# Optimization experiments

Hardware: AMD Instinct MI355X
Metric: run time of the kernel (lower is better)

Reference implementation:

```python
import jax, jax.numpy as jnp
import numpy as np

S = 17          # number of segment ids (0 = background, skipped)
MIN_H = 100.0   # HomographySmoothLoss.min_segment_pixels
MIN_V = 50.0    # ObjectVarianceLoss.min_segment_pixels
SUPPRESS = 0.1  # BoundaryAwareSmoothLoss.boundary_suppress


def _maxpool3(x):
    # torch F.max_pool2d(k=3, stride=1, pad=1) pads with -inf
    return jax.lax.reduce_window(x, -jnp.inf, jax.lax.max,
                                 (1, 1, 3, 3), (1, 1, 1, 1),
                                 ((0, 0), (0, 0), (1, 1), (1, 1)))


def _boundary_map(masks):
    lab = masks.astype(jnp.float32)[:, None]  # (B,1,H,W)
    dil = _maxpool3(lab)
    ero = -_maxpool3(-lab)
    return (dil != ero).astype(jnp.float32)


def _nearest(x, Ho, Wo):
    # torch F.interpolate(mode='nearest'): src = floor(dst * in/out)
    H, W = x.shape[-2], x.shape[-1]
    yi = (jnp.arange(Ho) * H) // Ho
    xi = (jnp.arange(Wo) * W) // Wo
    return x[..., yi, :][..., :, xi]


def _conv3(x, k):
    return jax.lax.conv_general_dilated(x, k, (1, 1), ((1, 1), (1, 1)),
                                        dimension_numbers=('NCHW', 'OIHW', 'NCHW'))


def _segment_losses(flow, masks):
    # Vectorized replacement of per-(batch,segment) python loops:
    # accumulate per-segment moments with segment_sum, then batched 3x3
    # normal-equation solves (equivalent to torch.lstsq affine fit).
    B, _, H, W = flow.shape
    NS = B * S
    xs = jnp.broadcast_to(jnp.arange(W, dtype=jnp.float32)[None, None, :], (B, H, W)).reshape(-1)
    ys = jnp.broadcast_to(jnp.arange(H, dtype=jnp.float32)[None, :, None], (B, H, W)).reshape(-1)
    u = flow[:, 0].reshape(-1)
    v = flow[:, 1].reshape(-1)
    seg = masks.reshape(-1)
    bidx = jnp.repeat(jnp.arange(B, dtype=jnp.int32), H * W)
    idx = bidx * S + seg                                  # global segment id
    ones = jnp.ones_like(xs)
    feats = jnp.stack([ones, xs, ys, xs * xs, xs * ys, ys * ys,
                       u, v, u * u, v * v, xs * u, ys * u, xs * v, ys * v], axis=1)
    sums = jax.ops.segment_sum(feats, idx, num_segments=NS)  # (NS,14)
    (n, Sx, Sy, Sxx, Sxy, Syy, Su, Sv, Suu, Svv,
     Sxu, Syu, Sxv, Syv) = [sums[:, i] for i in range(14)]
    segids = jnp.tile(jnp.arange(S), B)

    # ---- homography loss: per-segment affine least-squares fit ----
    valid_h = (segids != 0) & (n >= MIN_H)
    ATA = jnp.stack([jnp.stack([Sxx, Sxy, Sx], -1),
                     jnp.stack([Sxy, Syy, Sy], -1),
                     jnp.stack([Sx, Sy, n], -1)], axis=1)   # (NS,3,3)
    eye3 = jnp.eye(3, dtype=flow.dtype)
    ATA = jnp.where(valid_h[:, None, None], ATA, eye3)      # keep solve nonsingular
    ATb = jnp.stack([jnp.stack([Sxu, Sxv], -1),
                     jnp.stack([Syu, Syv], -1),
                     jnp.stack([Su, Sv], -1)], axis=1)      # (NS,3,2)
    ATb = jnp.where(valid_h[:, None, None], ATb, 0.0)
    params = jnp.linalg.solve(ATA, ATb)                     # (NS,3,2): [a,b,c] for u and v
    p = params[idx]                                         # (BHW,3,2) gather per pixel
    pred_u = xs * p[:, 0, 0] + ys * p[:, 1, 0] + p[:, 2, 0]
    pred_v = xs * p[:, 0, 1] + ys * p[:, 1, 1] + p[:, 2, 1]
    res = jnp.sqrt((u - pred_u) ** 2 + (v - pred_v) ** 2)
    res_mean = jax.ops.segment_sum(res, idx, num_segments=NS) / jnp.maximum(n, 1.0)
    nh = jnp.maximum(jnp.sum(valid_h), 1)
    homog = jnp.sum(res_mean * valid_h) / nh

    # ---- object variance loss (unbiased var, matches torch .var()) ----
    valid_v = (segids != 0) & (n >= MIN_V)
    nsafe = jnp.maximum(n, 2.0)
    var_u = (Suu - Su * Su / nsafe) / (nsafe - 1.0)
    var_v = (Svv - Sv * Sv / nsafe) / (nsafe - 1.0)
    nv = jnp.maximum(jnp.sum(valid_v), 1)
    ovar = jnp.sum((var_u + var_v) * valid_v) / nv
    return homog, ovar


def setup_inputs():
    key = jax.random.key(0)
    k1, k2, k3 = jax.random.split(key, 3)
    B, H, W = 8, 512, 1024
    flow = jax.random.normal(k1, (B, 2, H, W), jnp.float32)
    masks = jax.random.randint(k2, (B, H, W), 0, S).astype(jnp.int32)
    images = jax.random.uniform(k3, (B, 3, H, W), jnp.float32)
    return {"flow": flow, "masks": masks, "images": images}


def reference(flow, masks, images):
    boundary = _boundary_map(masks)                         # (B,1,H,W)
    homog, ovar = _segment_losses(flow, masks)

    # ---- boundary sharpness (sobel on flow magnitude) ----
    sobel_x = jnp.array([[-1., 0., 1.], [-2., 0., 2.], [-1., 0., 1.]], jnp.float32).reshape(1, 1, 3, 3)
    sobel_y = jnp.array([[-1., -2., -1.], [0., 0., 0.], [1., 2., 1.]], jnp.float32).reshape(1, 1, 3, 3)
    flow_mag = jnp.sqrt(jnp.sum(flow ** 2, axis=1, keepdims=True))
    fg = jnp.abs(_conv3(flow_mag, sobel_x)) + jnp.abs(_conv3(flow_mag, sobel_y))
    fg = fg / (jnp.max(fg) + 1e-6)
    bn = boundary / (jnp.max(boundary) + 1e-6)
    sharp = jnp.mean(bn * (1.0 - fg))

    # ---- boundary-aware edge-weighted smoothness ----
    flow_dx = flow[:, :, :, 1:] - flow[:, :, :, :-1]
    flow_dy = flow[:, :, 1:, :] - flow[:, :, :-1, :]
    g = jnp.mean(images, axis=1, keepdims=True)
    wx = jnp.exp(-jnp.abs(g[:, :, :, 1:] - g[:, :, :, :-1]) * 10.0)
    wy = jnp.exp(-jnp.abs(g[:, :, 1:, :] - g[:, :, :-1, :]) * 10.0)
    bx = _nearest(boundary, wx.shape[2], wx.shape[3])
    by = _nearest(boundary, wy.shape[2], wy.shape[3])
    wx = wx * (1.0 - (1.0 - SUPPRESS) * bx)
    wy = wy * (1.0 - (1.0 - SUPPRESS) * by)
    smooth = jnp.mean(jnp.abs(flow_dx) * wx) + jnp.mean(jnp.abs(flow_dy) * wy)

    # weights all 1.0; order: homography, boundary_sharpness, object_variance, boundary_smooth
    return jnp.stack([homog, sharp, ovar, smooth])
```

## Files before the change

### kernel.cpp

```cpp
#include <hip/hip_runtime.h>
#include <math.h>

#define BB 8
#define HH 512
#define WW 1024
#define HW (HH * WW)
#define NPIX (BB * HW)
#define NSEG 16
#define SUPPRESS 0.1f


__device__ __forceinline__ float wave_sum(float t) {
    #pragma unroll
    for (int off = 32; off > 0; off >>= 1) t += __shfl_down(t, off);
    return t;
}

#define REP8(M) M(0) M(1) M(2) M(3) M(4) M(5) M(6) M(7)

__global__ __launch_bounds__(64) void moments_kernel(
    const float* __restrict__ flow,
    const int*   __restrict__ masks,
    double* __restrict__ moments4)
{
    __shared__ float bins[9984];

    const int lane = threadIdx.x;
    const int bid  = blockIdx.x;
    const int colg = bid & 15;
    const int rowg = (bid >> 4) & 7;
    const int b    = bid >> 7;
    const int par  = bid & 3;

    const int c0 = colg * 64;
    const int r0 = rowg * 64;

    const float* fu = flow + (long long)b * (2LL * HW);
    const float* fv = fu + HW;
    const int*   mk = masks + (long long)b * HW;
    const int*   mrow = mk + r0 * WW + c0 + lane;
    const float* urow = fu + r0 * WW + c0 + lane;
    const float* vrow = fv + r0 * WW + c0 + lane;

    #pragma unroll
    for (int i = 0; i < 39; ++i)
        *(float4*)&bins[i * 256 + lane * 4] = make_float4(0.f, 0.f, 0.f, 0.f);

    int   m0 = mrow[0];
    float u0 = urow[0], v0 = vrow[0];
    int   m1 = mrow[WW];
    float u1 = urow[WW], v1 = vrow[WW];

    #pragma unroll 1
    for (int r = 0; r < 64; r += 2) {
        const int o2 = ((r + 2) & 63) * WW;
        const int o3 = ((r + 3) & 63) * WW;
        const int   m2 = mrow[o2];
        const float u2 = urow[o2], v2 = vrow[o2];
        const int   m3 = mrow[o3];
        const float u3 = urow[o3], v3 = vrow[o3];

        {
            const float y = (float)(r0 + r);
            float* bp = &bins[m0 * 576 + lane];
            float b0 = bp[0],   b1 = bp[64],  b2 = bp[128];
            float b3 = bp[192], b4 = bp[256], b5 = bp[320];
            float b6 = bp[384], b7 = bp[448], b8 = bp[512];
            b0 += 1.f;
            b1 += y;
            b2 = fmaf(y, y, b2);
            b3 += u0;
            b4 += v0;
            b5 = fmaf(u0, u0, b5);
            b6 = fmaf(v0, v0, b6);
            b7 = fmaf(y, u0, b7);
            b8 = fmaf(y, v0, b8);
            bp[0] = b0;   bp[64] = b1;  bp[128] = b2;
            bp[192] = b3; bp[256] = b4; bp[320] = b5;
            bp[384] = b6; bp[448] = b7; bp[512] = b8;
        }
        {
            const float y = (float)(r0 + r + 1);
            float* bp = &bins[m1 * 576 + lane];
            float b0 = bp[0],   b1 = bp[64],  b2 = bp[128];
            float b3 = bp[192], b4 = bp[256], b5 = bp[320];
            float b6 = bp[384], b7 = bp[448], b8 = bp[512];
            b0 += 1.f;
            b1 += y;
            b2 = fmaf(y, y, b2);
            b3 += u1;
            b4 += v1;
            b5 = fmaf(u1, u1, b5);
            b6 = fmaf(v1, v1, b6);
            b7 = fmaf(y, u1, b7);
            b8 = fmaf(y, v1, b8);
            bp[0] = b0;   bp[64] = b1;  bp[128] = b2;
            bp[192] = b3; bp[256] = b4; bp[320] = b5;
            bp[384] = b6; bp[448] = b7; bp[512] = b8;
        }
        m0 = m2; u0 = u2; v0 = v2;
        m1 = m3; u1 = u3; v1 = v3;
    }

    const unsigned long long SRC = 0x84736543210100ULL;
    const unsigned long long PW  = 0x01010000012010ULL;
    double* cell = moments4 + par * 1792 + b * 224;
    #pragma unroll 1
    for (int rp = 0; rp < 4; ++rp) {
        const int p   = rp * 64 + lane;
        const int act = (p < 224);
        const int pc  = act ? p : 0;
        const int segm = pc / 14;
        const int feat = pc - segm * 14;
        const int srcb = (int)((SRC >> (4 * feat)) & 15);
        const int pw   = (int)((PW  >> (4 * feat)) & 15);
        const float* bp = &bins[(segm + 1) * 576 + srcb * 64];
        float acc = 0.f;
        #pragma unroll 8
        for (int l0 = 0; l0 < 64; ++l0) {
            const int l = (l0 + lane) & 63;
            const float xv = (float)(c0 + l);
            const float w = (pw == 0) ? 1.f : ((pw == 1) ? xv : xv * xv);
            acc = fmaf(bp[l], w, acc);
        }
        if (act) atomicAdd(&cell[segm * 14 + feat], (double)acc);
    }
}

__global__ __launch_bounds__(256) void stencil_kernel(
    const float* __restrict__ flow,
    const int*   __restrict__ masks,
    const float* __restrict__ images,
    double* __restrict__ scal64,
    unsigned* __restrict__ maxfg64)
{
    __shared__ float         sm[4][1032];
    __shared__ unsigned char smask[4][1032];
    __shared__ float         sg[3][1024];
    __shared__ float         wred[4][5];

    const int tid = threadIdx.x;
    const int lane = tid & 63;
    const long long base = (long long)blockIdx.x * 2048;
    const int b  = (int)(base >> 19);
    const int h0 = (int)((base & (HW - 1)) >> 10);

    const float* fu = flow + (long long)b * (2LL * HW);
    const float* fv = fu + HW;
    const int*   mk = masks + (long long)b * HW;
    const float* i0 = images + (long long)b * (3LL * HW);
    const float* i1 = i0 + HW;
    const float* i2 = i1 + HW;

    const int c4 = tid * 4;
    #pragma unroll
    for (int r = 0; r < 4; ++r) {
        const int gr = h0 - 1 + r;
        const int mr = gr < 0 ? 0 : (gr > HH - 1 ? HH - 1 : gr);
        const int4 mv = *(const int4*)&mk[mr * WW + c4];
        uchar4 mb;
        mb.x = (unsigned char)mv.x; mb.y = (unsigned char)mv.y;
        mb.z = (unsigned char)mv.z; mb.w = (unsigned char)mv.w;
        *(uchar4*)&smask[r][4 + c4] = mb;

        float4 u4 = make_float4(0.f, 0.f, 0.f, 0.f);
        float4 v4 = make_float4(0.f, 0.f, 0.f, 0.f);
        if (gr >= 0 && gr <= HH - 1) {
            u4 = *(const float4*)&fu[gr * WW + c4];
            v4 = *(const float4*)&fv[gr * WW + c4];
        }
        float4 m4;
        m4.x = sqrtf(u4.x * u4.x + v4.x * v4.x);
        m4.y = sqrtf(u4.y * u4.y + v4.y * v4.y);
        m4.z = sqrtf(u4.z * u4.z + v4.z * v4.z);
        m4.w = sqrtf(u4.w * u4.w + v4.w * v4.w);
        *(float4*)&sm[r][4 + c4] = m4;
    }
    #pragma unroll
    for (int r = 0; r < 3; ++r) {
        const int gr = h0 + r;
        float4 g4 = make_float4(0.f, 0.f, 0.f, 0.f);
        if (gr <= HH - 1) {
            const float4 a  = *(const float4*)&i0[gr * WW + c4];
            const float4 bq = *(const float4*)&i1[gr * WW + c4];
            const float4 c  = *(const float4*)&i2[gr * WW + c4];
            g4.x = (a.x + bq.x + c.x) * (1.f / 3.f);
            g4.y = (a.y + bq.y + c.y) * (1.f / 3.f);
            g4.z = (a.z + bq.z + c.z) * (1.f / 3.f);
            g4.w = (a.w + bq.w + c.w) * (1.f / 3.f);
        }
        *(float4*)&sg[r][c4] = g4;
    }
    if (tid < 4) {
        const int gr = h0 - 1 + tid;
        const int mr = gr < 0 ? 0 : (gr > HH - 1 ? HH - 1 : gr);
        smask[tid][3]    = (unsigned char)mk[mr * WW + 0];
        smask[tid][1028] = (unsigned char)mk[mr * WW + WW - 1];
        sm[tid][3] = 0.f;
        sm[tid][1028] = 0.f;
    }
    __syncthreads();

    float a_dx = 0.f, a_dy = 0.f, a_sb = 0.f, a_sbf = 0.f, mfg = 0.f;

    #pragma unroll
    for (int it = 0; it < 8; ++it) {
        const int idx = it * 256 + tid;
        const int lr = idx >> 10;
        const int w  = idx & 1023;
        const int h  = h0 + lr;
        const int cc = 4 + w;

        const int segc = smask[lr + 1][cc];
        int bnd = (smask[lr][cc - 1] != segc) | (smask[lr][cc] != segc) |
                  (smask[lr][cc + 1] != segc) |
                  (smask[lr + 1][cc - 1] != segc) | (smask[lr + 1][cc + 1] != segc) |
                  (smask[lr + 2][cc - 1] != segc) | (smask[lr + 2][cc] != segc) |
                  (smask[lr + 2][cc + 1] != segc);

        const float t00 = sm[lr][cc - 1],     t01 = sm[lr][cc],     t02 = sm[lr][cc + 1];
        const float t10 = sm[lr + 1][cc - 1],                       t12 = sm[lr + 1][cc + 1];
        const float t20 = sm[lr + 2][cc - 1], t21 = sm[lr + 2][cc], t22 = sm[lr + 2][cc + 1];
        const float fgx = (t02 - t00) + 2.f * (t12 - t10) + (t22 - t20);
        const float fgy = (t20 + 2.f * t21 + t22) - (t00 + 2.f * t01 + t02);
        const float fgraw = fabsf(fgx) + fabsf(fgy);
        mfg = fmaxf(mfg, fgraw);
        if (bnd) { a_sb += 1.f; a_sbf += fgraw; }

        const int hw = h * WW + w;
        const float u = fu[hw], v = fv[hw];
        const float g0 = sg[lr][w];
        if (w < WW - 1) {
            const float wgt = expf(-fabsf(sg[lr][w + 1] - g0) * 10.f) * (bnd ? SUPPRESS : 1.f);
            a_dx += (fabsf(fu[hw + 1] - u) + fabsf(fv[hw + 1] - v)) * wgt;
        }
        if (h < HH - 1) {
            const float wgt = expf(-fabsf(sg[lr + 1][w] - g0) * 10.f) * (bnd ? SUPPRESS : 1.f);
            a_dy += (fabsf(fu[hw + WW] - u) + fabsf(fv[hw + WW] - v)) * wgt;
        }
    }

    for (int off = 32; off > 0; off >>= 1) {
        a_dx += __shfl_down(a_dx, off);
        a_dy += __shfl_down(a_dy, off);
        a_sb += __shfl_down(a_sb, off);
        a_sbf += __shfl_down(a_sbf, off);
        mfg = fmaxf(mfg, __shfl_down(mfg, off));
    }
    if (lane == 0) {
        const int wv = tid >> 6;
        wred[wv][0] = a_dx; wred[wv][1] = a_dy; wred[wv][2] = a_sb;
        wred[wv][3] = a_sbf; wred[wv][4] = mfg;
    }
    __syncthreads();
    if (tid == 0) {
        float dx = 0.f, dy = 0.f, sb = 0.f, sbf = 0.f, mf = 0.f;
        for (int i = 0; i < 4; ++i) {
            dx += wred[i][0]; dy += wred[i][1]; sb += wred[i][2];
            sbf += wred[i][3]; mf = fmaxf(mf, wred[i][4]);
        }
        const int sl = blockIdx.x & 63;
        atomicAdd(&scal64[sl * 4 + 0], (double)dx);
        atomicAdd(&scal64[sl * 4 + 1], (double)dy);
        atomicAdd(&scal64[sl * 4 + 2], (double)sb);
        atomicAdd(&scal64[sl * 4 + 3], (double)sbf);
        atomicMax(&maxfg64[sl], __float_as_uint(mf));
    }
}

__global__ __launch_bounds__(128) void solve_kernel(
    const double* __restrict__ moments4,
    float* __restrict__ params,
    int* __restrict__ valid,
    float* __restrict__ out)
{
    const int i = threadIdx.x;
    double m[14];
    #pragma unroll
    for (int k = 0; k < 14; ++k) {
        double s = 0.0;
        #pragma unroll
        for (int par = 0; par < 4; ++par) s += moments4[par * 1792 + i * 14 + k];
        m[k] = s;
    }
    const double n = m[0];
    const int vh = (n >= 100.0) ? 1 : 0;
    float p[6] = {0.f, 0.f, 0.f, 0.f, 0.f, 0.f};
    if (vh) {
        double A[3][3] = {{m[3], m[4], m[1]},
                          {m[4], m[5], m[2]},
                          {m[1], m[2], n}};
        double Bm[3][2] = {{m[10], m[12]},
                           {m[11], m[13]},
                           {m[6],  m[7]}};
        for (int k = 0; k < 3; ++k) {
            int piv = k; double mx = fabs(A[k][k]);
            for (int r = k + 1; r < 3; ++r) {
                double a = fabs(A[r][k]);
                if (a > mx) { mx = a; piv = r; }
            }
            if (piv != k) {
                for (int c = 0; c < 3; ++c) { double t = A[k][c]; A[k][c] = A[piv][c]; A[piv][c] = t; }
                for (int c = 0; c < 2; ++c) { double t = Bm[k][c]; Bm[k][c] = Bm[piv][c]; Bm[piv][c] = t; }
            }
            const double inv = 1.0 / A[k][k];
            for (int r = k + 1; r < 3; ++r) {
                const double f = A[r][k] * inv;
                for (int c = k; c < 3; ++c) A[r][c] -= f * A[k][c];
                Bm[r][0] -= f * Bm[k][0];
                Bm[r][1] -= f * Bm[k][1];
            }
        }
        double X[3][2];
        for (int c = 0; c < 2; ++c) {
            X[2][c] = Bm[2][c] / A[2][2];
            X[1][c] = (Bm[1][c] - A[1][2] * X[2][c]) / A[1][1];
            X[0][c] = (Bm[0][c] - A[0][1] * X[1][c] - A[0][2] * X[2][c]) / A[0][0];
        }
        p[0] = (float)X[0][0]; p[1] = (float)X[1][0]; p[2] = (float)X[2][0];
        p[3] = (float)X[0][1]; p[4] = (float)X[1][1]; p[5] = (float)X[2][1];
    }
    valid[i] = vh;
    for (int c = 0; c < 6; ++c) params[i * 6 + c] = p[c];

    const int vv = (n >= 50.0) ? 1 : 0;
    double var = 0.0;
    if (vv) {
        const double ns = (n > 2.0) ? n : 2.0;
        const double var_u = (m[8] - m[6] * m[6] / ns) / (ns - 1.0);
        const double var_v = (m[9] - m[7] * m[7] / ns) / (ns - 1.0);
        var = var_u + var_v;
    }
    __shared__ double svar[128];
    __shared__ int scnt[128];
    svar[i] = var; scnt[i] = vv;
    __syncthreads();
    for (int s = 64; s > 0; s >>= 1) {
        if (i < s) { svar[i] += svar[i + s]; scnt[i] += scnt[i + s]; }
        __syncthreads();
    }
    if (i == 0) out[2] = (float)(svar[0] / (double)(scnt[0] > 1 ? scnt[0] : 1));
}

__global__ __launch_bounds__(256) void pass2_kernel(
    const float* __restrict__ flow,
    const int*   __restrict__ masks,
    const float* __restrict__ params,
    double* __restrict__ res4)
{
    __shared__ float sp[17 * 6];

    const long long base = (long long)blockIdx.x * 4096;
    const int b      = (int)(base >> 19);
    const int hwbase = (int)(base & (HW - 1));
    const int tid    = threadIdx.x;
    const int lane   = tid & 63;

    if (tid < 6) sp[tid] = 0.f;
    if (tid < 96) sp[6 + tid] = params[b * 96 + tid];
    __syncthreads();

    const float* fu = flow + (long long)b * (2LL * HW);
    const float* fv = fu + HW;
    const int*   mk = masks + (long long)b * HW;

#define DECLR(i) float r_##i = 0.f;
    REP8(DECLR)
#define DECLR2(i) float q_##i = 0.f;
    REP8(DECLR2)

    #pragma unroll
    for (int it = 0; it < 4; ++it) {
        const int i4 = hwbase + it * 1024 + tid * 4;
        const int4   m4 = *(const int4*)&mk[i4];
        const float4 u4 = *(const float4*)&fu[i4];
        const float4 v4 = *(const float4*)&fv[i4];
        const int segs[4] = {m4.x, m4.y, m4.z, m4.w};
        const float us[4] = {u4.x, u4.y, u4.z, u4.w};
        const float vs[4] = {v4.x, v4.y, v4.z, v4.w};
        #pragma unroll
        for (int j = 0; j < 4; ++j) {
            const int seg = segs[j];
            const float* pf = &sp[seg * 6];
            const int hw = i4 + j;
            const float x = (float)(hw & 1023), y = (float)((hw & (HW - 1)) >> 10);
            const float du = us[j] - (x * pf[0] + y * pf[1] + pf[2]);
            const float dv = vs[j] - (x * pf[3] + y * pf[4] + pf[5]);
            const float r = sqrtf(du * du + dv * dv);
            const int sr = seg - 1;
#define STEPR(i) r_##i += (sr == i) ? r : 0.f;
            REP8(STEPR)
#define STEPR2(i) q_##i += (sr == 8 + i) ? r : 0.f;
            REP8(STEPR2)
        }
    }

    const int par = blockIdx.x & 3;
    double* rb = &res4[par * 128 + b * 16];
#define FINR(i) { const float s = wave_sum(r_##i); \
    if (lane == 0) atomicAdd(rb + i, (double)s); }
    REP8(FINR)
#define FINR2(i) { const float s = wave_sum(q_##i); \
    if (lane == 0) atomicAdd(rb + 8 + i, (double)s); }
    REP8(FINR2)
}

__global__ __launch_bounds__(128) void final_kernel(
    const double* __restrict__ moments4,
    const double* __restrict__ res4,
    const int*    __restrict__ valid,
    const double* __restrict__ scal64,
    const unsigned* __restrict__ maxfg64,
    float* __restrict__ out)
{
    const int i = threadIdx.x;
    double n = 0.0, rs = 0.0;
    #pragma unroll
    for (int par = 0; par < 4; ++par) {
        n  += moments4[par * 1792 + i * 14];
        rs += res4[par * 128 + i];
    }
    const int vh = valid[i];
    const double rm = vh ? rs / (n > 1.0 ? n : 1.0) : 0.0;
    __shared__ double sr[128];
    __shared__ int sc[128];
    sr[i] = rm; sc[i] = vh;
    __syncthreads();
    for (int s = 64; s > 0; s >>= 1) {
        if (i < s) { sr[i] += sr[i + s]; sc[i] += sc[i + s]; }
        __syncthreads();
    }
    if (i == 0) {
        out[0] = (float)(sr[0] / (double)(sc[0] > 1 ? sc[0] : 1));
        double dx = 0.0, dy = 0.0, sb = 0.0, sbf = 0.0;
        float mf = 0.f;
        for (int k = 0; k < 64; ++k) {
            dx += scal64[k * 4 + 0]; dy += scal64[k * 4 + 1];
            sb += scal64[k * 4 + 2]; sbf += scal64[k * 4 + 3];
            mf = fmaxf(mf, __uint_as_float(maxfg64[k]));
        }
        const double maxfg = (double)mf;
        const double maxb = (sb > 0.0) ? 1.0 : 0.0;
        out[1] = (float)((sb - sbf / (maxfg + 1e-6)) / (maxb + 1e-6) / (double)NPIX);
        const double smooth = dx / (double)(2LL * BB * HH * (WW - 1)) +
                              dy / (double)(2LL * BB * (HH - 1) * WW);
        out[3] = (float)smooth;
    }
}

extern "C" void kernel_launch(void* const* d_in, const int* in_sizes, int n_in,
                              void* d_out, int out_size, void* d_ws, size_t ws_size,
                              hipStream_t stream)
{
    const float* flow   = (const float*)d_in[0];
    const int*   masks  = (const int*)d_in[1];
    const float* images = (const float*)d_in[2];
    float* out = (float*)d_out;

    char* ws = (char*)d_ws;
    double*   moments4 = (double*)(ws);
    double*   res4     = (double*)(ws + 57344);
    double*   scal64   = (double*)(ws + 61440);
    unsigned* maxfg64  = (unsigned*)(ws + 63488);
    float*    params   = (float*)(ws + 63744);
    int*      valid    = (int*)(ws + 66816);

    hipMemsetAsync(d_ws, 0, 67584, stream);

    moments_kernel<<<dim3(1024), dim3(64), 0, stream>>>(flow, masks, moments4);
    stencil_kernel<<<dim3(NPIX / 2048), dim3(256), 0, stream>>>(
        flow, masks, images, scal64, maxfg64);
    solve_kernel<<<dim3(1), dim3(128), 0, stream>>>(moments4, params, valid, out);
    pass2_kernel<<<dim3(NPIX / 4096), dim3(256), 0, stream>>>(
        flow, masks, params, res4);
    final_kernel<<<dim3(1), dim3(128), 0, stream>>>(
        moments4, res4, valid, scal64, maxfg64, out);
}
```

Measured before the change: 119.7 us.

## Process four adjacent pixels per thread in stencil, reusing register-held flow and gray

The stencil loop now handles four consecutive columns per thread over two rows. The mask and magnitude neighbourhoods are read once into registers, and the mask bytes are packed into 64-bit words. The flow and gray values already loaded for the shared-memory fill are reused for the dx/dy terms, with a small shared edge buffer for the right neighbour, instead of re-reading flow from global memory per pixel. A launch-bounds occupancy hint is also added. The cost is higher register pressure per thread and less parallel slack per pixel.

```diff
diff --git a/kernel.cpp b/kernel.cpp
--- a/kernel.cpp
+++ b/kernel.cpp
@@ -127,7 +127,7 @@
     }
 }
 
-__global__ __launch_bounds__(256) void stencil_kernel(
+__global__ __launch_bounds__(256, 4) void stencil_kernel(
     const float* __restrict__ flow,
     const int*   __restrict__ masks,
     const float* __restrict__ images,
@@ -137,6 +137,8 @@
     __shared__ float         sm[4][1032];
     __shared__ unsigned char smask[4][1032];
     __shared__ float         sg[3][1024];
+    __shared__ float         ue[2][260];
+    __shared__ float         ve[2][260];
     __shared__ float         wred[4][5];
 
     const int tid = threadIdx.x;
@@ -153,6 +155,8 @@
     const float* i2 = i1 + HW;
 
     const int c4 = tid * 4;
+    float4 ur0, ur1, ur2, vr0, vr1, vr2;
+
     #pragma unroll
     for (int r = 0; r < 4; ++r) {
         const int gr = h0 - 1 + r;
@@ -175,7 +179,11 @@
         m4.z = sqrtf(u4.z * u4.z + v4.z * v4.z);
         m4.w = sqrtf(u4.w * u4.w + v4.w * v4.w);
         *(float4*)&sm[r][4 + c4] = m4;
-    }
+        if (r == 1) { ur0 = u4; vr0 = v4; }
+        else if (r == 2) { ur1 = u4; vr1 = v4; }
+        else if (r == 3) { ur2 = u4; vr2 = v4; }
+    }
+    float4 gr0, gr1, gr2;
     #pragma unroll
     for (int r = 0; r < 3; ++r) {
         const int gr = h0 + r;
@@ -190,7 +198,10 @@
             g4.w = (a.w + bq.w + c.w) * (1.f / 3.f);
         }
         *(float4*)&sg[r][c4] = g4;
-    }
+        if (r == 0) gr0 = g4; else if (r == 1) gr1 = g4; else gr2 = g4;
+    }
+    ue[0][tid] = ur0.x; ve[0][tid] = vr0.x;
+    ue[1][tid] = ur1.x; ve[1][tid] = vr1.x;
     if (tid < 4) {
         const int gr = h0 - 1 + tid;
         const int mr = gr < 0 ? 0 : (gr > HH - 1 ? HH - 1 : gr);
@@ -204,39 +215,65 @@
     float a_dx = 0.f, a_dy = 0.f, a_sb = 0.f, a_sbf = 0.f, mfg = 0.f;
 
     #pragma unroll
-    for (int it = 0; it < 8; ++it) {
-        const int idx = it * 256 + tid;
-        const int lr = idx >> 10;
-        const int w  = idx & 1023;
-        const int h  = h0 + lr;
-        const int cc = 4 + w;
-
-        const int segc = smask[lr + 1][cc];
-        int bnd = (smask[lr][cc - 1] != segc) | (smask[lr][cc] != segc) |
-                  (smask[lr][cc + 1] != segc) |
-                  (smask[lr + 1][cc - 1] != segc) | (smask[lr + 1][cc + 1] != segc) |
-                  (smask[lr + 2][cc - 1] != segc) | (smask[lr + 2][cc] != segc) |
-                  (smask[lr + 2][cc + 1] != segc);
-
-        const float t00 = sm[lr][cc - 1],     t01 = sm[lr][cc],     t02 = sm[lr][cc + 1];
-        const float t10 = sm[lr + 1][cc - 1],                       t12 = sm[lr + 1][cc + 1];
-        const float t20 = sm[lr + 2][cc - 1], t21 = sm[lr + 2][cc], t22 = sm[lr + 2][cc + 1];
-        const float fgx = (t02 - t00) + 2.f * (t12 - t10) + (t22 - t20);
-        const float fgy = (t20 + 2.f * t21 + t22) - (t00 + 2.f * t01 + t02);
-        const float fgraw = fabsf(fgx) + fabsf(fgy);
-        mfg = fmaxf(mfg, fgraw);
-        if (bnd) { a_sb += 1.f; a_sbf += fgraw; }
-
-        const int hw = h * WW + w;
-        const float u = fu[hw], v = fv[hw];
-        const float g0 = sg[lr][w];
-        if (w < WW - 1) {
-            const float wgt = expf(-fabsf(sg[lr][w + 1] - g0) * 10.f) * (bnd ? SUPPRESS : 1.f);
-            a_dx += (fabsf(fu[hw + 1] - u) + fabsf(fv[hw + 1] - v)) * wgt;
-        }
-        if (h < HH - 1) {
-            const float wgt = expf(-fabsf(sg[lr + 1][w] - g0) * 10.f) * (bnd ? SUPPRESS : 1.f);
-            a_dy += (fabsf(fu[hw + WW] - u) + fabsf(fv[hw + WW] - v)) * wgt;
+    for (int lr = 0; lr < 2; ++lr) {
+        const int h = h0 + lr;
+        float a[3][6];
+        unsigned long long kw[3];
+        #pragma unroll
+        for (int r = 0; r < 3; ++r) {
+            const int rr = lr + r;
+            const float4 own = *(const float4*)&sm[rr][4 + c4];
+            a[r][0] = sm[rr][3 + c4];
+            a[r][1] = own.x; a[r][2] = own.y; a[r][3] = own.z; a[r][4] = own.w;
+            a[r][5] = sm[rr][8 + c4];
+            const unsigned mpk = *(const unsigned*)&smask[rr][4 + c4];
+            kw[r] = (unsigned long long)smask[rr][3 + c4]
+                  | ((unsigned long long)mpk << 8)
+                  | ((unsigned long long)smask[rr][8 + c4] << 40);
+        }
+        const float4 gc = (lr == 0) ? gr0 : gr1;
+        const float4 gd4 = (lr == 0) ? gr1 : gr2;
+        const float gRn = (c4 + 4 < WW) ? sg[lr][c4 + 4] : 0.f;
+        const float gval[5] = {gc.x, gc.y, gc.z, gc.w, gRn};
+        const float4 uc4 = (lr == 0) ? ur0 : ur1;
+        const float4 vc4 = (lr == 0) ? vr0 : vr1;
+        const float4 ud4 = (lr == 0) ? ur1 : ur2;
+        const float4 vd4 = (lr == 0) ? vr1 : vr2;
+        const float uc[5] = {uc4.x, uc4.y, uc4.z, uc4.w, ue[lr][tid + 1]};
+        const float vc[5] = {vc4.x, vc4.y, vc4.z, vc4.w, ve[lr][tid + 1]};
+        const float ud[4] = {ud4.x, ud4.y, ud4.z, ud4.w};
+        const float vd[4] = {vd4.x, vd4.y, vd4.z, vd4.w};
+
+        #pragma unroll
+        for (int j = 0; j < 4; ++j) {
+            const int w = c4 + j;
+            const int cseg = (int)((kw[1] >> (8 * (j + 1))) & 255);
+            int bnd = (((kw[0] >> (8 * j)) & 255) != (unsigned)cseg)
+                    | (((kw[0] >> (8 * (j + 1))) & 255) != (unsigned)cseg)
+                    | (((kw[0] >> (8 * (j + 2))) & 255) != (unsigned)cseg)
+                    | (((kw[1] >> (8 * j)) & 255) != (unsigned)cseg)
+                    | (((kw[1] >> (8 * (j + 2))) & 255) != (unsigned)cseg)
+                    | (((kw[2] >> (8 * j)) & 255) != (unsigned)cseg)
+                    | (((kw[2] >> (8 * (j + 1))) & 255) != (unsigned)cseg)
+                    | (((kw[2] >> (8 * (j + 2))) & 255) != (unsigned)cseg);
+
+            const float fgx = (a[0][j + 2] - a[0][j]) + 2.f * (a[1][j + 2] - a[1][j]) +
+                              (a[2][j + 2] - a[2][j]);
+            const float fgy = (a[2][j] + 2.f * a[2][j + 1] + a[2][j + 2]) -
+                              (a[0][j] + 2.f * a[0][j + 1] + a[0][j + 2]);
+            const float fgraw = fabsf(fgx) + fabsf(fgy);
+            mfg = fmaxf(mfg, fgraw);
+            if (bnd) { a_sb += 1.f; a_sbf += fgraw; }
+
+            const float u = uc[j], v = vc[j], g0 = gval[j];
+            if (w < WW - 1) {
+                const float wgt = expf(-fabsf(gval[j + 1] - g0) * 10.f) * (bnd ? SUPPRESS : 1.f);
+                a_dx += (fabsf(uc[j + 1] - u) + fabsf(vc[j + 1] - v)) * wgt;
+            }
+            if (h < HH - 1) {
+                const float wgt = expf(-fabsf(gd4.x * 0.f + ((const float*)&gd4)[j] - g0) * 10.f) * (bnd ? SUPPRESS : 1.f);
+                a_dy += (fabsf(ud[j] - u) + fabsf(vd[j] - v)) * wgt;
+            }
         }
     }
 
```

New measurement: 108.4 us. 1.1x faster.

## Fuse segment-moment histogram and boundary stencil into one sliding-window kernel

Applied to the files above, without the earlier changes.

Merges the per-segment moments kernel and the boundary/smoothness stencil kernel into one 64-thread kernel. Each wave walks 64 rows over a 62-column tile with one-column halos, keeping a 3-row register window and using lane shuffles for horizontal neighbours. This avoids reading flow and masks twice and drops a kernel launch. In exchange each block now reads images in a column-strided pattern, works on only 62 of 64 lanes, and is limited to one 64-thread wave with a large LDS footprint, which may cut occupancy.

```diff
diff --git a/kernel.cpp b/kernel.cpp
--- a/kernel.cpp
+++ b/kernel.cpp
@@ -18,88 +18,131 @@
 
 #define REP8(M) M(0) M(1) M(2) M(3) M(4) M(5) M(6) M(7)
 
-__global__ __launch_bounds__(64) void moments_kernel(
+__global__ __launch_bounds__(64) void fused_kernel(
     const float* __restrict__ flow,
     const int*   __restrict__ masks,
-    double* __restrict__ moments4)
+    const float* __restrict__ images,
+    double* __restrict__ moments4,
+    double* __restrict__ scal64,
+    unsigned* __restrict__ maxfg64)
 {
     __shared__ float bins[9984];
 
     const int lane = threadIdx.x;
     const int bid  = blockIdx.x;
-    const int colg = bid & 15;
-    const int rowg = (bid >> 4) & 7;
-    const int b    = bid >> 7;
+    const int colg = bid % 17;
+    const int rest = bid / 17;
+    const int rowg = rest & 7;
+    const int b    = rest >> 3;
     const int par  = bid & 3;
 
-    const int c0 = colg * 64;
-    const int r0 = rowg * 64;
+    const int c0  = colg * 62;
+    const int r0  = rowg * 64;
+    const int col = c0 + lane - 1;
+    const int gc  = col < 0 ? 0 : (col > WW - 1 ? WW - 1 : col);
+    const bool colOK = (col >= 0 && col <= WW - 1);
+    const bool act   = (lane >= 1 && lane <= 62 && col <= WW - 1);
 
     const float* fu = flow + (long long)b * (2LL * HW);
     const float* fv = fu + HW;
     const int*   mk = masks + (long long)b * HW;
-    const int*   mrow = mk + r0 * WW + c0 + lane;
-    const float* urow = fu + r0 * WW + c0 + lane;
-    const float* vrow = fv + r0 * WW + c0 + lane;
+    const float* i0 = images + (long long)b * (3LL * HW);
+    const float* i1 = i0 + HW;
+    const float* i2 = i1 + HW;
 
     #pragma unroll
     for (int i = 0; i < 39; ++i)
         *(float4*)&bins[i * 256 + lane * 4] = make_float4(0.f, 0.f, 0.f, 0.f);
 
-    int   m0 = mrow[0];
-    float u0 = urow[0], v0 = vrow[0];
-    int   m1 = mrow[WW];
-    float u1 = urow[WW], v1 = vrow[WW];
+    float mp = 0.f, mc = 0.f, mn = 0.f;
+    float mLp = 0.f, mLc = 0.f, mLn = 0.f, mRp = 0.f, mRc = 0.f, mRn = 0.f;
+    int   kp = 0, kc = 0, kn = 0;
+    int   kLp = 0, kLc = 0, kLn = 0, kRp = 0, kRc = 0, kRn = 0;
+    float gcur = 0.f, gnxt = 0.f, gRc = 0.f, gRn = 0.f;
+    float ucur = 0.f, unxt = 0.f, uRc = 0.f, uRn = 0.f;
+    float vcur = 0.f, vnxt = 0.f, vRc = 0.f, vRn = 0.f;
+
+#define LDROW(rr, MR, UR, VR, GR) { \
+    const int rcl = (rr) < 0 ? 0 : ((rr) > HH - 1 ? HH - 1 : (rr)); \
+    const int off = rcl * WW + gc; \
+    MR = mk[off]; UR = fu[off]; VR = fv[off]; \
+    GR = (i0[off] + i1[off] + i2[off]) * (1.f / 3.f); }
+
+#define MAKEWIN(rr, MR, UR, VR, GR) { \
+    const bool rOK = ((rr) >= 0 && (rr) <= HH - 1); \
+    mn = (rOK && colOK) ? sqrtf(UR * UR + VR * VR) : 0.f; \
+    kn = MR & 255; \
+    gnxt = GR; unxt = UR; vnxt = VR; \
+    mLn = __shfl_up(mn, 1);  mRn = __shfl_down(mn, 1); \
+    kLn = __shfl_up(kn, 1);  kRn = __shfl_down(kn, 1); \
+    gRn = __shfl_down(gnxt, 1); \
+    uRn = __shfl_down(unxt, 1); vRn = __shfl_down(vnxt, 1); }
+
+#define SHIFTW { \
+    mp = mc; mc = mn; mLp = mLc; mLc = mLn; mRp = mRc; mRc = mRn; \
+    kp = kc; kc = kn; kLp = kLc; kLc = kLn; kRp = kRc; kRc = kRn; \
+    gcur = gnxt; gRc = gRn; ucur = unxt; uRc = uRn; vcur = vnxt; vRc = vRn; }
+
+    int mrA, mrB, mrC; float urA, vrA, grA, urB, vrB, grB, urC, vrC, grC;
+    LDROW(r0 - 1, mrA, urA, vrA, grA)
+    MAKEWIN(r0 - 1, mrA, urA, vrA, grA)
+    SHIFTW
+    LDROW(r0, mrA, urA, vrA, grA)
+    MAKEWIN(r0, mrA, urA, vrA, grA)
+    SHIFTW
+    LDROW(r0 + 1, mrA, urA, vrA, grA)
+    LDROW(r0 + 2, mrB, urB, vrB, grB)
+
+    float a_dx = 0.f, a_dy = 0.f, a_sb = 0.f, a_sbf = 0.f, mfg = 0.f;
 
     #pragma unroll 1
-    for (int r = 0; r < 64; r += 2) {
-        const int o2 = ((r + 2) & 63) * WW;
-        const int o3 = ((r + 3) & 63) * WW;
-        const int   m2 = mrow[o2];
-        const float u2 = urow[o2], v2 = vrow[o2];
-        const int   m3 = mrow[o3];
-        const float u3 = urow[o3], v3 = vrow[o3];
-
+    for (int ri = 0; ri < 64; ++ri) {
+        LDROW(r0 + ri + 3, mrC, urC, vrC, grC)
+        MAKEWIN(r0 + ri + 1, mrA, urA, vrA, grA)
+
+        const int rc = r0 + ri;
+        const int bnd = (kLp != kc) | (kp != kc) | (kRp != kc) |
+                        (kLc != kc) | (kRc != kc) |
+                        (kLn != kc) | (kn != kc) | (kRn != kc);
+        const float fgx = (mRp - mLp) + 2.f * (mRc - mLc) + (mRn - mLn);
+        const float fgy = (mLn + 2.f * mn + mRn) - (mLp + 2.f * mp + mRp);
+        const float fgraw = fabsf(fgx) + fabsf(fgy);
+        if (act) {
+            mfg = fmaxf(mfg, fgraw);
+            if (bnd) { a_sb += 1.f; a_sbf += fgraw; }
+            if (col < WW - 1) {
+                const float wgt = expf(-fabsf(gRc - gcur) * 10.f) * (bnd ? SUPPRESS : 1.f);
+                a_dx += (fabsf(uRc - ucur) + fabsf(vRc - vcur)) * wgt;
+            }
+            if (rc < HH - 1) {
+                const float wgt = expf(-fabsf(gnxt - gcur) * 10.f) * (bnd ? SUPPRESS : 1.f);
+                a_dy += (fabsf(unxt - ucur) + fabsf(vnxt - vcur)) * wgt;
+            }
+        }
         {
-            const float y = (float)(r0 + r);
-            float* bp = &bins[m0 * 576 + lane];
+            const int seg = act ? kc : 0;
+            float* bp = &bins[seg * 576 + lane];
+            const float y = (float)rc;
             float b0 = bp[0],   b1 = bp[64],  b2 = bp[128];
             float b3 = bp[192], b4 = bp[256], b5 = bp[320];
             float b6 = bp[384], b7 = bp[448], b8 = bp[512];
             b0 += 1.f;
             b1 += y;
             b2 = fmaf(y, y, b2);
-            b3 += u0;
-            b4 += v0;
-            b5 = fmaf(u0, u0, b5);
-            b6 = fmaf(v0, v0, b6);
-            b7 = fmaf(y, u0, b7);
-            b8 = fmaf(y, v0, b8);
+            b3 += ucur;
+            b4 += vcur;
+            b5 = fmaf(ucur, ucur, b5);
+            b6 = fmaf(vcur, vcur, b6);
+            b7 = fmaf(y, ucur, b7);
+            b8 = fmaf(y, vcur, b8);
             bp[0] = b0;   bp[64] = b1;  bp[128] = b2;
             bp[192] = b3; bp[256] = b4; bp[320] = b5;
             bp[384] = b6; bp[448] = b7; bp[512] = b8;
         }
-        {
-            const float y = (float)(r0 + r + 1);
-            float* bp = &bins[m1 * 576 + lane];
-            float b0 = bp[0],   b1 = bp[64],  b2 = bp[128];
-            float b3 = bp[192], b4 = bp[256], b5 = bp[320];
-            float b6 = bp[384], b7 = bp[448], b8 = bp[512];
-            b0 += 1.f;
-            b1 += y;
-            b2 = fmaf(y, y, b2);
-            b3 += u1;
-            b4 += v1;
-            b5 = fmaf(u1, u1, b5);
-            b6 = fmaf(v1, v1, b6);
-            b7 = fmaf(y, u1, b7);
-            b8 = fmaf(y, v1, b8);
-            bp[0] = b0;   bp[64] = b1;  bp[128] = b2;
-            bp[192] = b3; bp[256] = b4; bp[320] = b5;
-            bp[384] = b6; bp[448] = b7; bp[512] = b8;
-        }
-        m0 = m2; u0 = u2; v0 = v2;
-        m1 = m3; u1 = u3; v1 = v3;
+
+        SHIFTW
+        mrA = mrB; urA = urB; vrA = vrB; grA = grB;
+        mrB = mrC; urB = urC; vrB = vrC; grB = grC;
     }
 
     const unsigned long long SRC = 0x84736543210100ULL;
@@ -108,8 +151,8 @@
     #pragma unroll 1
     for (int rp = 0; rp < 4; ++rp) {
         const int p   = rp * 64 + lane;
-        const int act = (p < 224);
-        const int pc  = act ? p : 0;
+        const int iac = (p < 224);
+        const int pc  = iac ? p : 0;
         const int segm = pc / 14;
         const int feat = pc - segm * 14;
         const int srcb = (int)((SRC >> (4 * feat)) & 15);
@@ -119,152 +162,26 @@
         #pragma unroll 8
         for (int l0 = 0; l0 < 64; ++l0) {
             const int l = (l0 + lane) & 63;
-            const float xv = (float)(c0 + l);
+            const float xv = (float)(c0 + l - 1);
             const float w = (pw == 0) ? 1.f : ((pw == 1) ? xv : xv * xv);
             acc = fmaf(bp[l], w, acc);
         }
-        if (act) atomicAdd(&cell[segm * 14 + feat], (double)acc);
-    }
-}
-
-__global__ __launch_bounds__(256) void stencil_kernel(
-    const float* __restrict__ flow,
-    const int*   __restrict__ masks,
-    const float* __restrict__ images,
-    double* __restrict__ scal64,
-    unsigned* __restrict__ maxfg64)
-{
-    __shared__ float         sm[4][1032];
-    __shared__ unsigned char smask[4][1032];
-    __shared__ float         sg[3][1024];
-    __shared__ float         wred[4][5];
-
-    const int tid = threadIdx.x;
-    const int lane = tid & 63;
-    const long long base = (long long)blockIdx.x * 2048;
-    const int b  = (int)(base >> 19);
-    const int h0 = (int)((base & (HW - 1)) >> 10);
-
-    const float* fu = flow + (long long)b * (2LL * HW);
-    const float* fv = fu + HW;
-    const int*   mk = masks + (long long)b * HW;
-    const float* i0 = images + (long long)b * (3LL * HW);
-    const float* i1 = i0 + HW;
-    const float* i2 = i1 + HW;
-
-    const int c4 = tid * 4;
-    #pragma unroll
-    for (int r = 0; r < 4; ++r) {
-        const int gr = h0 - 1 + r;
-        const int mr = gr < 0 ? 0 : (gr > HH - 1 ? HH - 1 : gr);
-        const int4 mv = *(const int4*)&mk[mr * WW + c4];
-        uchar4 mb;
-        mb.x = (unsigned char)mv.x; mb.y = (unsigned char)mv.y;
-        mb.z = (unsigned char)mv.z; mb.w = (unsigned char)mv.w;
-        *(uchar4*)&smask[r][4 + c4] = mb;
-
-        float4 u4 = make_float4(0.f, 0.f, 0.f, 0.f);
-        float4 v4 = make_float4(0.f, 0.f, 0.f, 0.f);
-        if (gr >= 0 && gr <= HH - 1) {
-            u4 = *(const float4*)&fu[gr * WW + c4];
-            v4 = *(const float4*)&fv[gr * WW + c4];
-        }
-        float4 m4;
-        m4.x = sqrtf(u4.x * u4.x + v4.x * v4.x);
-        m4.y = sqrtf(u4.y * u4.y + v4.y * v4.y);
-        m4.z = sqrtf(u4.z * u4.z + v4.z * v4.z);
-        m4.w = sqrtf(u4.w * u4.w + v4.w * v4.w);
-        *(float4*)&sm[r][4 + c4] = m4;
-    }
-    #pragma unroll
-    for (int r = 0; r < 3; ++r) {
-        const int gr = h0 + r;
-        float4 g4 = make_float4(0.f, 0.f, 0.f, 0.f);
-        if (gr <= HH - 1) {
-            const float4 a  = *(const float4*)&i0[gr * WW + c4];
-            const float4 bq = *(const float4*)&i1[gr * WW + c4];
-            const float4 c  = *(const float4*)&i2[gr * WW + c4];
-            g4.x = (a.x + bq.x + c.x) * (1.f / 3.f);
-            g4.y = (a.y + bq.y + c.y) * (1.f / 3.f);
-            g4.z = (a.z + bq.z + c.z) * (1.f / 3.f);
-            g4.w = (a.w + bq.w + c.w) * (1.f / 3.f);
-        }
-        *(float4*)&sg[r][c4] = g4;
-    }
-    if (tid < 4) {
-        const int gr = h0 - 1 + tid;
-        const int mr = gr < 0 ? 0 : (gr > HH - 1 ? HH - 1 : gr);
-        smask[tid][3]    = (unsigned char)mk[mr * WW + 0];
-        smask[tid][1028] = (unsigned char)mk[mr * WW + WW - 1];
-        sm[tid][3] = 0.f;
-        sm[tid][1028] = 0.f;
-    }
-    __syncthreads();
-
-    float a_dx = 0.f, a_dy = 0.f, a_sb = 0.f, a_sbf = 0.f, mfg = 0.f;
-
-    #pragma unroll
-    for (int it = 0; it < 8; ++it) {
-        const int idx = it * 256 + tid;
-        const int lr = idx >> 10;
-        const int w  = idx & 1023;
-        const int h  = h0 + lr;
-        const int cc = 4 + w;
-
-        const int segc = smask[lr + 1][cc];
-        int bnd = (smask[lr][cc - 1] != segc) | (smask[lr][cc] != segc) |
-                  (smask[lr][cc + 1] != segc) |
-                  (smask[lr + 1][cc - 1] != segc) | (smask[lr + 1][cc + 1] != segc) |
-                  (smask[lr + 2][cc - 1] != segc) | (smask[lr + 2][cc] != segc) |
-                  (smask[lr + 2][cc + 1] != segc);
-
-        const float t00 = sm[lr][cc - 1],     t01 = sm[lr][cc],     t02 = sm[lr][cc + 1];
-        const float t10 = sm[lr + 1][cc - 1],                       t12 = sm[lr + 1][cc + 1];
-        const float t20 = sm[lr + 2][cc - 1], t21 = sm[lr + 2][cc], t22 = sm[lr + 2][cc + 1];
-        const float fgx = (t02 - t00) + 2.f * (t12 - t10) + (t22 - t20);
-        const float fgy = (t20 + 2.f * t21 + t22) - (t00 + 2.f * t01 + t02);
-        const float fgraw = fabsf(fgx) + fabsf(fgy);
-        mfg = fmaxf(mfg, fgraw);
-        if (bnd) { a_sb += 1.f; a_sbf += fgraw; }
-
-        const int hw = h * WW + w;
-        const float u = fu[hw], v = fv[hw];
-        const float g0 = sg[lr][w];
-        if (w < WW - 1) {
-            const float wgt = expf(-fabsf(sg[lr][w + 1] - g0) * 10.f) * (bnd ? SUPPRESS : 1.f);
-            a_dx += (fabsf(fu[hw + 1] - u) + fabsf(fv[hw + 1] - v)) * wgt;
-        }
-        if (h < HH - 1) {
-            const float wgt = expf(-fabsf(sg[lr + 1][w] - g0) * 10.f) * (bnd ? SUPPRESS : 1.f);
-            a_dy += (fabsf(fu[hw + WW] - u) + fabsf(fv[hw + WW] - v)) * wgt;
-        }
-    }
-
-    for (int off = 32; off > 0; off >>= 1) {
-        a_dx += __shfl_down(a_dx, off);
-        a_dy += __shfl_down(a_dy, off);
-        a_sb += __shfl_down(a_sb, off);
-        a_sbf += __shfl_down(a_sbf, off);
-        mfg = fmaxf(mfg, __shfl_down(mfg, off));
-    }
+        if (iac) atomicAdd(&cell[segm * 14 + feat], (double)acc);
+    }
+
+    a_dx = wave_sum(a_dx);
+    a_dy = wave_sum(a_dy);
+    a_sb = wave_sum(a_sb);
+    a_sbf = wave_sum(a_sbf);
+    #pragma unroll
+    for (int off = 32; off > 0; off >>= 1) mfg = fmaxf(mfg, __shfl_down(mfg, off));
     if (lane == 0) {
-        const int wv = tid >> 6;
-        wred[wv][0] = a_dx; wred[wv][1] = a_dy; wred[wv][2] = a_sb;
-        wred[wv][3] = a_sbf; wred[wv][4] = mfg;
-    }
-    __syncthreads();
-    if (tid == 0) {
-        float dx = 0.f, dy = 0.f, sb = 0.f, sbf = 0.f, mf = 0.f;
-        for (int i = 0; i < 4; ++i) {
-            dx += wred[i][0]; dy += wred[i][1]; sb += wred[i][2];
-            sbf += wred[i][3]; mf = fmaxf(mf, wred[i][4]);
-        }
-        const int sl = blockIdx.x & 63;
-        atomicAdd(&scal64[sl * 4 + 0], (double)dx);
-        atomicAdd(&scal64[sl * 4 + 1], (double)dy);
-        atomicAdd(&scal64[sl * 4 + 2], (double)sb);
-        atomicAdd(&scal64[sl * 4 + 3], (double)sbf);
-        atomicMax(&maxfg64[sl], __float_as_uint(mf));
+        const int sl = bid & 63;
+        atomicAdd(&scal64[sl * 4 + 0], (double)a_dx);
+        atomicAdd(&scal64[sl * 4 + 1], (double)a_dy);
+        atomicAdd(&scal64[sl * 4 + 2], (double)a_sb);
+        atomicAdd(&scal64[sl * 4 + 3], (double)a_sbf);
+        atomicMax(&maxfg64[sl], __float_as_uint(mfg));
     }
 }
 
@@ -467,9 +384,8 @@
 
     hipMemsetAsync(d_ws, 0, 67584, stream);
 
-    moments_kernel<<<dim3(1024), dim3(64), 0, stream>>>(flow, masks, moments4);
-    stencil_kernel<<<dim3(NPIX / 2048), dim3(256), 0, stream>>>(
-        flow, masks, images, scal64, maxfg64);
+    fused_kernel<<<dim3(8 * 8 * 17), dim3(64), 0, stream>>>(
+        flow, masks, images, moments4, scal64, maxfg64);
     solve_kernel<<<dim3(1), dim3(128), 0, stream>>>(moments4, params, valid, out);
     pass2_kernel<<<dim3(NPIX / 4096), dim3(256), 0, stream>>>(
         flow, masks, params, res4);
```

Result: slower. 140.7 us (+17.5%).
